# Kernel tuning notes

Hardware: AMD Instinct MI355X
Metric: run time of the kernel (lower is better)

The kernel has to match this reference:

```python
import jax, jax.numpy as jnp
import numpy as np

D_MODEL = 1024
N_HEAD = 16

def setup_inputs() -> dict:
    key = jax.random.key(0)
    ks = jax.random.split(key, 11)
    B, S, D = 2, 2048, D_MODEL
    s = 1.0 / np.sqrt(D)
    inp = {
        'q': jax.random.normal(ks[0], (B, S, D), jnp.float32),
        'k': jax.random.normal(ks[1], (B, S, D), jnp.float32),
        'v': jax.random.normal(ks[2], (B, S, D), jnp.float32),
        'w_q': jax.random.normal(ks[3], (D, D), jnp.float32) * s,
        'b_q': jnp.zeros((D,), jnp.float32),
        'w_k': jax.random.normal(ks[4], (D, D), jnp.float32) * s,
        'b_k': jnp.zeros((D,), jnp.float32),
        'w_v': jax.random.normal(ks[5], (D, D), jnp.float32) * s,
        'b_v': jnp.zeros((D,), jnp.float32),
        'w_o': jax.random.normal(ks[6], (D, D), jnp.float32) * s,
        'b_o': jnp.zeros((D,), jnp.float32),
    }
    return inp

def _split_heads(x):
    B, S, D = x.shape
    return x.reshape(B, S, N_HEAD, D // N_HEAD).transpose(0, 2, 1, 3)  # [B,H,S,d]

def reference(q, k, v, w_q, b_q, w_k, b_k, w_v, b_v, w_o, b_o):
    # Linear projections (torch Linear: x @ W.T + b)
    qh = _split_heads(q @ w_q.T + b_q)
    kh = _split_heads(k @ w_k.T + b_k)
    vh = _split_heads(v @ w_v.T + b_v)
    d_k = qh.shape[-1]
    scores = jnp.einsum('bhqd,bhkd->bhqk', qh, kh) / jnp.sqrt(jnp.float32(d_k))
    attn = jax.nn.softmax(scores, axis=-1)
    out = jnp.einsum('bhqk,bhkd->bhqd', attn, vh)  # [B,H,S,d]
    B, H, S, d = out.shape
    out = out.transpose(0, 2, 1, 3).reshape(B, S, H * d)
    return out @ w_o.T + b_o
```

## Files before the change

kernel.cpp:

```cpp
#include <hip/hip_runtime.h>
#include <hip/hip_bf16.h>

typedef __hip_bfloat16 bf16;
typedef short bf16x8 __attribute__((ext_vector_type(8)));
typedef float f32x4 __attribute__((ext_vector_type(4)));

#define D_MODEL 1024
#define SEQ     2048
#define NHEAD   16
#define DHEAD   64
#define BATCH   2
#define MROWS   (BATCH*SEQ)
#define LOG2E   1.4426950408889634f

__device__ __forceinline__ void lds_dma16(const bf16* g, bf16* l) {
  __builtin_amdgcn_global_load_lds(
      (const __attribute__((address_space(1))) void*)g,
      (__attribute__((address_space(3))) void*)l, 16, 0, 0);
}

__device__ __forceinline__ uint4 pack8_f32(const float4 x0, const float4 x1) {
  union { uint4 q; bf16 h[8]; } pk;
  pk.h[0]=__float2bfloat16(x0.x); pk.h[1]=__float2bfloat16(x0.y);
  pk.h[2]=__float2bfloat16(x0.z); pk.h[3]=__float2bfloat16(x0.w);
  pk.h[4]=__float2bfloat16(x1.x); pk.h[5]=__float2bfloat16(x1.y);
  pk.h[6]=__float2bfloat16(x1.z); pk.h[7]=__float2bfloat16(x1.w);
  return pk.q;
}

__global__ void probe_dtype(const void* __restrict__ w, int* __restrict__ flag) {
  __shared__ int cnt;
  const int tid = threadIdx.x;
  if (tid == 0) cnt = 0;
  __syncthreads();
  float v = ((const float*)w)[tid];
  bool sane = (v == v) && fabsf(v) < 1e3f && fabsf(v) > 1e-8f;
  if (sane) atomicAdd(&cnt, 1);
  __syncthreads();
  if (tid == 0) *flag = (cnt >= 128) ? 1 : 0;
}

__global__ __launch_bounds__(256) void convert7(
    const void* s0, const void* s1, const void* s2, const void* s3,
    const void* s4, const void* s5, const void* s6,
    bf16* d0, bf16* d1, bf16* d2, bf16* d3, bf16* d4, bf16* d5, bf16* d6,
    const int* __restrict__ dflag)
{
  const void* S[7] = {s0,s1,s2,s3,s4,s5,s6};
  bf16*       D[7] = {d0,d1,d2,d3,d4,d5,d6};
  const int z = blockIdx.y;
  const int n8 = (z < 3) ? (MROWS*D_MODEL/8) : (D_MODEL*D_MODEL/8);
  const bool is32 = (*dflag != 0);
  for (int i = blockIdx.x*256 + threadIdx.x; i < n8; i += 512*256) {
    if (is32) {
      float4 a = ((const float4*)S[z])[2*i];
      float4 b = ((const float4*)S[z])[2*i+1];
      ((uint4*)D[z])[i] = pack8_f32(a, b);
    } else {
      ((uint4*)D[z])[i] = ((const uint4*)S[z])[i];
    }
  }
}

__global__ __launch_bounds__(256) void gemm3_dma(
    const bf16* A0, const bf16* A1, const bf16* A2,
    const bf16* W0, const bf16* W1, const bf16* W2,
    const void* B0, const void* B1, const void* B2,
    bf16* C0, bf16* C1, bf16* C2, const int* __restrict__ dflag)
{
  __shared__ __align__(16) bf16 As[4*128*8];
  __shared__ __align__(16) bf16 Ws[4*128*8];
  const int z = blockIdx.z;
  const bf16* A = (z == 0) ? A0 : (z == 1) ? A1 : A2;
  const bf16* W = (z == 0) ? W0 : (z == 1) ? W1 : W2;
  const void* Bv = (z == 0) ? B0 : (z == 1) ? B1 : B2;
  bf16* C = (z == 0) ? C0 : (z == 1) ? C1 : C2;
  const float scale = (z == 0) ? 0.125f*LOG2E : 1.0f;
  const int K = D_MODEL, N = D_MODEL;
  const bool is32 = (*dflag != 0);
  const int tid  = threadIdx.x;
  const int lane = tid & 63, wave = tid >> 6;
  const int wm   = wave >> 1, wn = wave & 1;
  const int quad = lane >> 4, l16 = lane & 15;
  const int row0 = blockIdx.y * 128, col0 = blockIdx.x * 128;

  const f32x4 zero = {0.f, 0.f, 0.f, 0.f};
  f32x4 acc[4][4];
  #pragma unroll
  for (int i = 0; i < 4; ++i)
    #pragma unroll
    for (int j = 0; j < 4; ++j) acc[i][j] = zero;

  for (int k0 = 0; k0 < K; k0 += 32) {
    __syncthreads();
    #pragma unroll
    for (int t = 0; t < 2; ++t) {
      int s = t*256 + tid;
      int g = s >> 7, r = s & 127;
      lds_dma16(A + (size_t)(row0 + r)*K + k0 + g*8, &As[s*8]);
      lds_dma16(W + (size_t)(col0 + r)*K + k0 + g*8, &Ws[s*8]);
    }
    __syncthreads();
    bf16x8 af[4], wf[4];
    #pragma unroll
    for (int mt = 0; mt < 4; ++mt)
      af[mt] = *(const bf16x8*)&As[(quad*128 + wm*64 + mt*16 + l16)*8];
    #pragma unroll
    for (int nt = 0; nt < 4; ++nt)
      wf[nt] = *(const bf16x8*)&Ws[(quad*128 + wn*64 + nt*16 + l16)*8];
    #pragma unroll
    for (int mt = 0; mt < 4; ++mt)
      #pragma unroll
      for (int nt = 0; nt < 4; ++nt)
        acc[mt][nt] = __builtin_amdgcn_mfma_f32_16x16x32_bf16(af[mt], wf[nt], acc[mt][nt], 0, 0, 0);
  }

  #pragma unroll
  for (int nt = 0; nt < 4; ++nt) {
    int c = col0 + wn*64 + nt*16 + l16;
    float bv = is32 ? ((const float*)Bv)[c] : __bfloat162float(((const bf16*)Bv)[c]);
    #pragma unroll
    for (int mt = 0; mt < 4; ++mt) {
      int r = row0 + wm*64 + mt*16 + quad*4;
      #pragma unroll
      for (int j = 0; j < 4; ++j)
        C[(size_t)(r + j)*N + c] = __float2bfloat16((acc[mt][nt][j] + bv) * scale);
    }
  }
}

__global__ __launch_bounds__(256) void gemm_out_dma(
    const bf16* __restrict__ A, const bf16* __restrict__ W,
    const void* __restrict__ Bv, void* __restrict__ C,
    const int* __restrict__ dflag)
{
  __shared__ __align__(16) bf16 As[4*128*8];
  __shared__ __align__(16) bf16 Ws[4*64*8];
  const int K = D_MODEL, N = D_MODEL;
  const bool is32 = (*dflag != 0);
  const int tid  = threadIdx.x;
  const int lane = tid & 63, wave = tid >> 6;
  const int wm   = wave >> 1, wn = wave & 1;
  const int quad = lane >> 4, l16 = lane & 15;
  const int row0 = blockIdx.y * 128, col0 = blockIdx.x * 64;

  const f32x4 zero = {0.f, 0.f, 0.f, 0.f};
  f32x4 acc[4][2];
  #pragma unroll
  for (int i = 0; i < 4; ++i)
    #pragma unroll
    for (int j = 0; j < 2; ++j) acc[i][j] = zero;

  for (int k0 = 0; k0 < K; k0 += 32) {
    __syncthreads();
    #pragma unroll
    for (int t = 0; t < 2; ++t) {
      int s = t*256 + tid;
      int g = s >> 7, r = s & 127;
      lds_dma16(A + (size_t)(row0 + r)*K + k0 + g*8, &As[s*8]);
    }
    {
      int g = tid >> 6, r = tid & 63;
      lds_dma16(W + (size_t)(col0 + r)*K + k0 + g*8, &Ws[tid*8]);
    }
    __syncthreads();
    bf16x8 af[4], wf[2];
    #pragma unroll
    for (int mt = 0; mt < 4; ++mt)
      af[mt] = *(const bf16x8*)&As[(quad*128 + wm*64 + mt*16 + l16)*8];
    #pragma unroll
    for (int nt = 0; nt < 2; ++nt)
      wf[nt] = *(const bf16x8*)&Ws[(quad*64 + wn*32 + nt*16 + l16)*8];
    #pragma unroll
    for (int mt = 0; mt < 4; ++mt)
      #pragma unroll
      for (int nt = 0; nt < 2; ++nt)
        acc[mt][nt] = __builtin_amdgcn_mfma_f32_16x16x32_bf16(af[mt], wf[nt], acc[mt][nt], 0, 0, 0);
  }

  #pragma unroll
  for (int nt = 0; nt < 2; ++nt) {
    int c = col0 + wn*32 + nt*16 + l16;
    float bv = is32 ? ((const float*)Bv)[c] : __bfloat162float(((const bf16*)Bv)[c]);
    #pragma unroll
    for (int mt = 0; mt < 4; ++mt) {
      int r = row0 + wm*64 + mt*16 + quad*4;
      #pragma unroll
      for (int j = 0; j < 4; ++j) {
        float outv = acc[mt][nt][j] + bv;
        size_t idx = (size_t)(r + j)*N + c;
        if (is32) ((float*)C)[idx] = outv;
        else      ((bf16*)C)[idx]  = __float2bfloat16(outv);
      }
    }
  }
}

__global__ __launch_bounds__(256) void gemm3_fused(
    const void* A0, const void* A1, const void* A2,
    const void* W0, const void* W1, const void* W2,
    const void* B0, const void* B1, const void* B2,
    bf16* C0, bf16* C1, bf16* C2, const int* __restrict__ dflag)
{
  __shared__ __align__(16) bf16 As[4*128*8];
  __shared__ __align__(16) bf16 Ws[4*128*8];
  const int z = blockIdx.z;
  const void* A = (z == 0) ? A0 : (z == 1) ? A1 : A2;
  const void* W = (z == 0) ? W0 : (z == 1) ? W1 : W2;
  const void* Bv = (z == 0) ? B0 : (z == 1) ? B1 : B2;
  bf16* C = (z == 0) ? C0 : (z == 1) ? C1 : C2;
  const float scale = (z == 0) ? 0.125f*LOG2E : 1.0f;
  const int K = D_MODEL, N = D_MODEL;
  const bool is32 = (*dflag != 0);
  const int tid  = threadIdx.x;
  const int lane = tid & 63, wave = tid >> 6;
  const int wm   = wave >> 1, wn = wave & 1;
  const int quad = lane >> 4, l16 = lane & 15;
  const int row0 = blockIdx.y * 128, col0 = blockIdx.x * 128;

  const f32x4 zero = {0.f, 0.f, 0.f, 0.f};
  f32x4 acc[4][4];
  #pragma unroll
  for (int i = 0; i < 4; ++i)
    #pragma unroll
    for (int j = 0; j < 4; ++j) acc[i][j] = zero;

  for (int k0 = 0; k0 < K; k0 += 32) {
    __syncthreads();
    #pragma unroll
    for (int t = 0; t < 2; ++t) {
      int s = t*256 + tid;
      int g = s >> 7, r = s & 127;
      size_t offA = (size_t)(row0 + r)*K + k0 + g*8;
      size_t offW = (size_t)(col0 + r)*K + k0 + g*8;
      if (is32) {
        const float* Af = (const float*)A + offA;
        *(uint4*)&As[s*8] = pack8_f32(((const float4*)Af)[0], ((const float4*)Af)[1]);
        const float* Wf = (const float*)W + offW;
        *(uint4*)&Ws[s*8] = pack8_f32(((const float4*)Wf)[0], ((const float4*)Wf)[1]);
      } else {
        *(uint4*)&As[s*8] = *(const uint4*)((const bf16*)A + offA);
        *(uint4*)&Ws[s*8] = *(const uint4*)((const bf16*)W + offW);
      }
    }
    __syncthreads();
    bf16x8 af[4], wf[4];
    #pragma unroll
    for (int mt = 0; mt < 4; ++mt)
      af[mt] = *(const bf16x8*)&As[(quad*128 + wm*64 + mt*16 + l16)*8];
    #pragma unroll
    for (int nt = 0; nt < 4; ++nt)
      wf[nt] = *(const bf16x8*)&Ws[(quad*128 + wn*64 + nt*16 + l16)*8];
    #pragma unroll
    for (int mt = 0; mt < 4; ++mt)
      #pragma unroll
      for (int nt = 0; nt < 4; ++nt)
        acc[mt][nt] = __builtin_amdgcn_mfma_f32_16x16x32_bf16(af[mt], wf[nt], acc[mt][nt], 0, 0, 0);
  }
  #pragma unroll
  for (int nt = 0; nt < 4; ++nt) {
    int c = col0 + wn*64 + nt*16 + l16;
    float bv = is32 ? ((const float*)Bv)[c] : __bfloat162float(((const bf16*)Bv)[c]);
    #pragma unroll
    for (int mt = 0; mt < 4; ++mt) {
      int r = row0 + wm*64 + mt*16 + quad*4;
      #pragma unroll
      for (int j = 0; j < 4; ++j)
        C[(size_t)(r + j)*N + c] = __float2bfloat16((acc[mt][nt][j] + bv) * scale);
    }
  }
}

__global__ __launch_bounds__(256) void gemm_out_fused(
    const bf16* __restrict__ A, const void* __restrict__ W,
    const void* __restrict__ Bv, void* __restrict__ C,
    const int* __restrict__ dflag)
{
  __shared__ __align__(16) bf16 As[4*128*8];
  __shared__ __align__(16) bf16 Ws[4*64*8];
  const int K = D_MODEL, N = D_MODEL;
  const bool is32 = (*dflag != 0);
  const int tid  = threadIdx.x;
  const int lane = tid & 63, wave = tid >> 6;
  const int wm   = wave >> 1, wn = wave & 1;
  const int quad = lane >> 4, l16 = lane & 15;
  const int row0 = blockIdx.y * 128, col0 = blockIdx.x * 64;

  const f32x4 zero = {0.f, 0.f, 0.f, 0.f};
  f32x4 acc[4][2];
  #pragma unroll
  for (int i = 0; i < 4; ++i)
    #pragma unroll
    for (int j = 0; j < 2; ++j) acc[i][j] = zero;

  for (int k0 = 0; k0 < K; k0 += 32) {
    __syncthreads();
    #pragma unroll
    for (int t = 0; t < 2; ++t) {
      int s = t*256 + tid;
      int g = s >> 7, r = s & 127;
      *(uint4*)&As[s*8] = *(const uint4*)(A + (size_t)(row0 + r)*K + k0 + g*8);
    }
    {
      int g = tid >> 6, r = tid & 63;
      size_t offW = (size_t)(col0 + r)*K + k0 + g*8;
      if (is32) {
        const float* Wf = (const float*)W + offW;
        *(uint4*)&Ws[tid*8] = pack8_f32(((const float4*)Wf)[0], ((const float4*)Wf)[1]);
      } else {
        *(uint4*)&Ws[tid*8] = *(const uint4*)((const bf16*)W + offW);
      }
    }
    __syncthreads();
    bf16x8 af[4], wf[2];
    #pragma unroll
    for (int mt = 0; mt < 4; ++mt)
      af[mt] = *(const bf16x8*)&As[(quad*128 + wm*64 + mt*16 + l16)*8];
    #pragma unroll
    for (int nt = 0; nt < 2; ++nt)
      wf[nt] = *(const bf16x8*)&Ws[(quad*64 + wn*32 + nt*16 + l16)*8];
    #pragma unroll
    for (int mt = 0; mt < 4; ++mt)
      #pragma unroll
      for (int nt = 0; nt < 2; ++nt)
        acc[mt][nt] = __builtin_amdgcn_mfma_f32_16x16x32_bf16(af[mt], wf[nt], acc[mt][nt], 0, 0, 0);
  }
  #pragma unroll
  for (int nt = 0; nt < 2; ++nt) {
    int c = col0 + wn*32 + nt*16 + l16;
    float bv = is32 ? ((const float*)Bv)[c] : __bfloat162float(((const bf16*)Bv)[c]);
    #pragma unroll
    for (int mt = 0; mt < 4; ++mt) {
      int r = row0 + wm*64 + mt*16 + quad*4;
      #pragma unroll
      for (int j = 0; j < 4; ++j) {
        float outv = acc[mt][nt][j] + bv;
        size_t idx = (size_t)(r + j)*N + c;
        if (is32) ((float*)C)[idx] = outv;
        else      ((bf16*)C)[idx]  = __float2bfloat16(outv);
      }
    }
  }
}

__global__ __launch_bounds__(512, 4) void attn_fused(
    const bf16* __restrict__ Qp, const bf16* __restrict__ Kp,
    const bf16* __restrict__ Vp, bf16* __restrict__ Ao)
{
  __shared__ __align__(16) bf16 UN[128*128];
  __shared__ __align__(16) bf16 Ks[8*128*8];
  __shared__ __align__(16) bf16 Vt[64*16*8];

  const int tid  = threadIdx.x;
  const int lane = tid & 63, wave = tid >> 6;
  const int quad = lane >> 4, l16 = lane & 15;
  const int qt = blockIdx.x, h = blockIdx.y, b = blockIdx.z;
  const int q0 = qt * 128;
  const bf16* Qb = Qp + ((size_t)b*SEQ + q0)*D_MODEL + h*DHEAD;
  const bf16* Kb = Kp + (size_t)b*SEQ*D_MODEL + h*DHEAD;
  const bf16* Vb = Vp + (size_t)b*SEQ*D_MODEL + h*DHEAD;

  #pragma unroll
  for (int t = 0; t < 2; ++t) {
    int s = t*512 + tid;
    int g = s >> 7, r = s & 127;
    lds_dma16(Qb + (size_t)r*D_MODEL + g*8, &UN[s*8]);
  }
  __syncthreads();

  const int wq0 = wave * 16;
  const int q   = wq0 + l16;
  bf16x8 qa[2];
  #pragma unroll
  for (int ks = 0; ks < 2; ++ks)
    qa[ks] = *(const bf16x8*)&UN[((ks*4 + quad)*128 + q)*8];
  __syncthreads();
  bf16* Ps = UN;
  const int swz = (l16 & 7) << 1;

  const f32x4 zero = {0.f, 0.f, 0.f, 0.f};
  f32x4 acc_o[4];
  #pragma unroll
  for (int dt = 0; dt < 4; ++dt) acc_o[dt] = zero;
  float m_s = -1e30f, l_s = 0.f;

  for (int kt = 0; kt < SEQ/128; ++kt) {
    const bf16* Kt_ = Kb + (size_t)kt*128*D_MODEL;
    const bf16* Vs_ = Vb + (size_t)kt*128*D_MODEL;
    #pragma unroll
    for (int t = 0; t < 2; ++t) {
      int s = t*512 + tid;
      int g = s >> 7, kk = s & 127;
      lds_dma16(Kt_ + (size_t)kk*D_MODEL + g*8, &Ks[s*8]);
    }
    #pragma unroll
    for (int t = 0; t < 2; ++t) {
      int c = t*512 + tid;
      int key = c >> 3, g8 = c & 7;
      uint4 raw = *(const uint4*)(Vs_ + (size_t)key*D_MODEL + g8*8);
      const bf16* e = (const bf16*)&raw;
      int gk = key >> 3, kb_i = key & 7;
      #pragma unroll
      for (int i = 0; i < 8; ++i) {
        int n = g8*8 + i;
        int sw = (gk + n + (n >> 3)) & 15;
        Vt[(n*16 + sw)*8 + kb_i] = e[i];
      }
    }
    __syncthreads();

    f32x4 sc[8];
    #pragma unroll
    for (int kt2 = 0; kt2 < 8; ++kt2) sc[kt2] = zero;
    #pragma unroll
    for (int ks = 0; ks < 2; ++ks) {
      bf16x8 kf[8];
      #pragma unroll
      for (int kt2 = 0; kt2 < 8; ++kt2)
        kf[kt2] = *(const bf16x8*)&Ks[((ks*4 + quad)*128 + kt2*16 + l16)*8];
      #pragma unroll
      for (int kt2 = 0; kt2 < 8; ++kt2)
        sc[kt2] = __builtin_amdgcn_mfma_f32_16x16x32_bf16(kf[kt2], qa[ks], sc[kt2], 0, 0, 0);
    }

    float vmax = -1e30f;
    #pragma unroll
    for (int kt2 = 0; kt2 < 8; ++kt2) {
      f32x4 s4 = sc[kt2];
      vmax = fmaxf(vmax, fmaxf(fmaxf(s4[0], s4[1]), fmaxf(s4[2], s4[3])));
    }
    vmax = fmaxf(vmax, __shfl_xor(vmax, 16));
    vmax = fmaxf(vmax, __shfl_xor(vmax, 32));
    float mnew  = fmaxf(m_s, vmax);
    float alpha = __builtin_amdgcn_exp2f(m_s - mnew);
    float rs = 0.f;
    #pragma unroll
    for (int kt2 = 0; kt2 < 8; ++kt2) {
      float p0 = __builtin_amdgcn_exp2f(sc[kt2][0] - mnew);
      float p1 = __builtin_amdgcn_exp2f(sc[kt2][1] - mnew);
      float p2 = __builtin_amdgcn_exp2f(sc[kt2][2] - mnew);
      float p3 = __builtin_amdgcn_exp2f(sc[kt2][3] - mnew);
      rs += (p0 + p1) + (p2 + p3);
      union { uint2 u; bf16 hh[4]; } pk;
      pk.hh[0] = __float2bfloat16(p0); pk.hh[1] = __float2bfloat16(p1);
      pk.hh[2] = __float2bfloat16(p2); pk.hh[3] = __float2bfloat16(p3);
      int phys = (kt2*4 + quad) ^ swz;
      *(uint2*)&Ps[q*128 + phys*4] = pk.u;
    }
    rs += __shfl_xor(rs, 16);
    rs += __shfl_xor(rs, 32);
    l_s = l_s*alpha + rs;
    m_s = mnew;
    #pragma unroll
    for (int dt = 0; dt < 4; ++dt) acc_o[dt] = acc_o[dt] * alpha;

    #pragma unroll
    for (int ks2 = 0; ks2 < 4; ++ks2) {
      bf16x8 vf[4], pa;
      #pragma unroll
      for (int dt = 0; dt < 4; ++dt) {
        int n = dt*16 + l16;
        int sw = (ks2*4 + quad + n + (n >> 3)) & 15;
        vf[dt] = *(const bf16x8*)&Vt[(n*16 + sw)*8];
      }
      int phys = (ks2*8 + quad*2) ^ swz;
      pa = *(const bf16x8*)&Ps[q*128 + phys*4];
      #pragma unroll
      for (int dt = 0; dt < 4; ++dt)
        acc_o[dt] = __builtin_amdgcn_mfma_f32_16x16x32_bf16(vf[dt], pa, acc_o[dt], 0, 0, 0);
    }
    __syncthreads();
  }

  bf16* Ob = Ao + ((size_t)b*SEQ + q0)*D_MODEL + h*DHEAD;
  float inv = 1.f / l_s;
  #pragma unroll
  for (int dt = 0; dt < 4; ++dt) {
    union { uint2 u; bf16 hh[4]; } pk;
    #pragma unroll
    for (int j = 0; j < 4; ++j) pk.hh[j] = __float2bfloat16(acc_o[dt][j] * inv);
    *(uint2*)(Ob + (size_t)q*D_MODEL + dt*16 + quad*4) = pk.u;
  }
}

extern "C" void kernel_launch(void* const* d_in, const int* in_sizes, int n_in,
                              void* d_out, int out_size, void* d_ws, size_t ws_size,
                              hipStream_t stream) {
  const void* q   = d_in[0];
  const void* k   = d_in[1];
  const void* v   = d_in[2];
  const void* w_q = d_in[3];
  const void* b_q = d_in[4];
  const void* w_k = d_in[5];
  const void* b_k = d_in[6];
  const void* w_v = d_in[7];
  const void* b_v = d_in[8];
  const void* w_o = d_in[9];
  const void* b_o = d_in[10];

  const size_t nbuf  = (size_t)MROWS * D_MODEL;
  const size_t wbuf  = (size_t)D_MODEL * D_MODEL;
  int* flag = (int*)d_ws;

  dim3 blk(256);
  probe_dtype<<<1, 256, 0, stream>>>(w_q, flag);

  const size_t needA = 256 + 3*nbuf*2 + 4*wbuf*2 + nbuf*2;
  if (ws_size >= needA) {
    bf16* qc  = (bf16*)((char*)d_ws + 256);
    bf16* kc  = qc  + nbuf;
    bf16* vc  = kc  + nbuf;
    bf16* wqc = vc  + nbuf;
    bf16* wkc = wqc + wbuf;
    bf16* wvc = wkc + wbuf;
    bf16* woc = wvc + wbuf;
    bf16* Qp  = woc + wbuf;
    bf16* Kp  = (bf16*)d_out;
    bf16* Vp  = Kp + nbuf;
    bf16* Ao  = Qp;

    dim3 gc(512, 7);
    convert7<<<gc, blk, 0, stream>>>(q, k, v, w_q, w_k, w_v, w_o,
                                     qc, kc, vc, wqc, wkc, wvc, woc, flag);
    dim3 g3(D_MODEL/128, MROWS/128, 3);
    gemm3_dma<<<g3, blk, 0, stream>>>(qc, kc, vc, wqc, wkc, wvc,
                                      b_q, b_k, b_v, Qp, Kp, Vp, flag);
    dim3 ga(SEQ/128, NHEAD, BATCH);
    attn_fused<<<ga, dim3(512), 0, stream>>>(Qp, Kp, Vp, Ao);
    dim3 go(D_MODEL/64, MROWS/128);
    gemm_out_dma<<<go, blk, 0, stream>>>(Ao, woc, b_o, d_out, flag);
  } else {
    bf16* Qp = (bf16*)((char*)d_ws + 256);
    bf16* Vp = Qp + nbuf;
    bf16* Kp = (bf16*)d_out;
    bf16* Ao = Qp;
    dim3 g3(D_MODEL/128, MROWS/128, 3);
    gemm3_fused<<<g3, blk, 0, stream>>>(q, k, v, w_q, w_k, w_v,
                                        b_q, b_k, b_v, Qp, Kp, Vp, flag);
    dim3 ga(SEQ/128, NHEAD, BATCH);
    attn_fused<<<ga, dim3(512), 0, stream>>>(Qp, Kp, Vp, Ao);
    dim3 go(D_MODEL/64, MROWS/128);
    gemm_out_fused<<<go, blk, 0, stream>>>(Ao, w_o, b_o, d_out, flag);
  }
}
```

Measured before the change: 314.1 us.

## Write V projection transposed, double GEMM K-step, drop dtype probe

The V projection epilogue now writes V in a transposed [batch, feature, seq] layout. The attention kernel can then load V rows with vector loads straight into the swizzled LDS tile instead of scattering single elements. The DMA GEMMs stage 64-wide K chunks per barrier pair instead of 32, halving the number of syncs. The runtime dtype probe kernel and its flag branches are removed by assuming fp32 inputs, and the attention kernel's launch-bounds occupancy hint is dropped. The costs are larger LDS tiles and transposed stores from the GEMM epilogue that are only partially coalesced.

```diff
diff --git a/kernel.cpp b/kernel.cpp
--- a/kernel.cpp
+++ b/kernel.cpp
@@ -28,56 +28,35 @@
   return pk.q;
 }
 
-__global__ void probe_dtype(const void* __restrict__ w, int* __restrict__ flag) {
-  __shared__ int cnt;
-  const int tid = threadIdx.x;
-  if (tid == 0) cnt = 0;
-  __syncthreads();
-  float v = ((const float*)w)[tid];
-  bool sane = (v == v) && fabsf(v) < 1e3f && fabsf(v) > 1e-8f;
-  if (sane) atomicAdd(&cnt, 1);
-  __syncthreads();
-  if (tid == 0) *flag = (cnt >= 128) ? 1 : 0;
-}
-
 __global__ __launch_bounds__(256) void convert7(
-    const void* s0, const void* s1, const void* s2, const void* s3,
-    const void* s4, const void* s5, const void* s6,
-    bf16* d0, bf16* d1, bf16* d2, bf16* d3, bf16* d4, bf16* d5, bf16* d6,
-    const int* __restrict__ dflag)
+    const float* s0, const float* s1, const float* s2, const float* s3,
+    const float* s4, const float* s5, const float* s6,
+    bf16* d0, bf16* d1, bf16* d2, bf16* d3, bf16* d4, bf16* d5, bf16* d6)
 {
-  const void* S[7] = {s0,s1,s2,s3,s4,s5,s6};
-  bf16*       D[7] = {d0,d1,d2,d3,d4,d5,d6};
+  const float* S[7] = {s0,s1,s2,s3,s4,s5,s6};
+  bf16*        D[7] = {d0,d1,d2,d3,d4,d5,d6};
   const int z = blockIdx.y;
   const int n8 = (z < 3) ? (MROWS*D_MODEL/8) : (D_MODEL*D_MODEL/8);
-  const bool is32 = (*dflag != 0);
   for (int i = blockIdx.x*256 + threadIdx.x; i < n8; i += 512*256) {
-    if (is32) {
-      float4 a = ((const float4*)S[z])[2*i];
-      float4 b = ((const float4*)S[z])[2*i+1];
-      ((uint4*)D[z])[i] = pack8_f32(a, b);
-    } else {
-      ((uint4*)D[z])[i] = ((const uint4*)S[z])[i];
-    }
+    float4 a = ((const float4*)S[z])[2*i];
+    float4 b = ((const float4*)S[z])[2*i+1];
+    ((uint4*)D[z])[i] = pack8_f32(a, b);
   }
 }
 
 __global__ __launch_bounds__(256) void gemm3_dma(
     const bf16* A0, const bf16* A1, const bf16* A2,
     const bf16* W0, const bf16* W1, const bf16* W2,
-    const void* B0, const void* B1, const void* B2,
-    bf16* C0, bf16* C1, bf16* C2, const int* __restrict__ dflag)
+    const float* B0, const float* B1, const float* B2,
+    bf16* C0, bf16* C1, bf16* VpT)
 {
-  __shared__ __align__(16) bf16 As[4*128*8];
-  __shared__ __align__(16) bf16 Ws[4*128*8];
+  __shared__ __align__(16) bf16 As[8*128*8];
+  __shared__ __align__(16) bf16 Ws[8*128*8];
   const int z = blockIdx.z;
   const bf16* A = (z == 0) ? A0 : (z == 1) ? A1 : A2;
   const bf16* W = (z == 0) ? W0 : (z == 1) ? W1 : W2;
-  const void* Bv = (z == 0) ? B0 : (z == 1) ? B1 : B2;
-  bf16* C = (z == 0) ? C0 : (z == 1) ? C1 : C2;
-  const float scale = (z == 0) ? 0.125f*LOG2E : 1.0f;
+  const float* Bv = (z == 0) ? B0 : (z == 1) ? B1 : B2;
   const int K = D_MODEL, N = D_MODEL;
-  const bool is32 = (*dflag != 0);
   const int tid  = threadIdx.x;
   const int lane = tid & 63, wave = tid >> 6;
   const int wm   = wave >> 1, wn = wave & 1;
@@ -91,53 +70,75 @@
     #pragma unroll
     for (int j = 0; j < 4; ++j) acc[i][j] = zero;
 
-  for (int k0 = 0; k0 < K; k0 += 32) {
-    __syncthreads();
-    #pragma unroll
-    for (int t = 0; t < 2; ++t) {
+  for (int k0 = 0; k0 < K; k0 += 64) {
+    __syncthreads();
+    #pragma unroll
+    for (int t = 0; t < 4; ++t) {
       int s = t*256 + tid;
       int g = s >> 7, r = s & 127;
       lds_dma16(A + (size_t)(row0 + r)*K + k0 + g*8, &As[s*8]);
       lds_dma16(W + (size_t)(col0 + r)*K + k0 + g*8, &Ws[s*8]);
     }
     __syncthreads();
-    bf16x8 af[4], wf[4];
-    #pragma unroll
-    for (int mt = 0; mt < 4; ++mt)
-      af[mt] = *(const bf16x8*)&As[(quad*128 + wm*64 + mt*16 + l16)*8];
-    #pragma unroll
-    for (int nt = 0; nt < 4; ++nt)
-      wf[nt] = *(const bf16x8*)&Ws[(quad*128 + wn*64 + nt*16 + l16)*8];
-    #pragma unroll
-    for (int mt = 0; mt < 4; ++mt)
+    #pragma unroll
+    for (int ks = 0; ks < 2; ++ks) {
+      bf16x8 af[4], wf[4];
+      #pragma unroll
+      for (int mt = 0; mt < 4; ++mt)
+        af[mt] = *(const bf16x8*)&As[((ks*4 + quad)*128 + wm*64 + mt*16 + l16)*8];
       #pragma unroll
       for (int nt = 0; nt < 4; ++nt)
-        acc[mt][nt] = __builtin_amdgcn_mfma_f32_16x16x32_bf16(af[mt], wf[nt], acc[mt][nt], 0, 0, 0);
-  }
-
-  #pragma unroll
-  for (int nt = 0; nt < 4; ++nt) {
-    int c = col0 + wn*64 + nt*16 + l16;
-    float bv = is32 ? ((const float*)Bv)[c] : __bfloat162float(((const bf16*)Bv)[c]);
-    #pragma unroll
-    for (int mt = 0; mt < 4; ++mt) {
-      int r = row0 + wm*64 + mt*16 + quad*4;
-      #pragma unroll
-      for (int j = 0; j < 4; ++j)
-        C[(size_t)(r + j)*N + c] = __float2bfloat16((acc[mt][nt][j] + bv) * scale);
+        wf[nt] = *(const bf16x8*)&Ws[((ks*4 + quad)*128 + wn*64 + nt*16 + l16)*8];
+      #pragma unroll
+      for (int mt = 0; mt < 4; ++mt)
+        #pragma unroll
+        for (int nt = 0; nt < 4; ++nt)
+          acc[mt][nt] = __builtin_amdgcn_mfma_f32_16x16x32_bf16(af[mt], wf[nt], acc[mt][nt], 0, 0, 0);
+    }
+  }
+
+  if (z < 2) {
+    bf16* C = (z == 0) ? C0 : C1;
+    const float scale = (z == 0) ? 0.125f*LOG2E : 1.0f;
+    #pragma unroll
+    for (int nt = 0; nt < 4; ++nt) {
+      int c = col0 + wn*64 + nt*16 + l16;
+      float bv = Bv[c];
+      #pragma unroll
+      for (int mt = 0; mt < 4; ++mt) {
+        int r = row0 + wm*64 + mt*16 + quad*4;
+        #pragma unroll
+        for (int j = 0; j < 4; ++j)
+          C[(size_t)(r + j)*N + c] = __float2bfloat16((acc[mt][nt][j] + bv) * scale);
+      }
+    }
+  } else {
+    const int bb = row0 >> 11;
+    const int sbase = (row0 & 2047) + wm*64;
+    #pragma unroll
+    for (int nt = 0; nt < 4; ++nt) {
+      int c = col0 + wn*64 + nt*16 + l16;
+      float bv = Bv[c];
+      bf16* col = VpT + (size_t)((bb << 10) + c) * SEQ;
+      #pragma unroll
+      for (int mt = 0; mt < 4; ++mt) {
+        int s = sbase + mt*16 + quad*4;
+        union { uint2 u; bf16 h[4]; } pk;
+        #pragma unroll
+        for (int j = 0; j < 4; ++j) pk.h[j] = __float2bfloat16(acc[mt][nt][j] + bv);
+        *(uint2*)(col + s) = pk.u;
+      }
     }
   }
 }
 
 __global__ __launch_bounds__(256) void gemm_out_dma(
     const bf16* __restrict__ A, const bf16* __restrict__ W,
-    const void* __restrict__ Bv, void* __restrict__ C,
-    const int* __restrict__ dflag)
+    const float* __restrict__ Bv, float* __restrict__ C)
 {
-  __shared__ __align__(16) bf16 As[4*128*8];
-  __shared__ __align__(16) bf16 Ws[4*64*8];
+  __shared__ __align__(16) bf16 As[8*128*8];
+  __shared__ __align__(16) bf16 Ws[8*64*8];
   const int K = D_MODEL, N = D_MODEL;
-  const bool is32 = (*dflag != 0);
   const int tid  = threadIdx.x;
   const int lane = tid & 63, wave = tid >> 6;
   const int wm   = wave >> 1, wn = wave & 1;
@@ -151,67 +152,65 @@
     #pragma unroll
     for (int j = 0; j < 2; ++j) acc[i][j] = zero;
 
-  for (int k0 = 0; k0 < K; k0 += 32) {
-    __syncthreads();
-    #pragma unroll
-    for (int t = 0; t < 2; ++t) {
+  for (int k0 = 0; k0 < K; k0 += 64) {
+    __syncthreads();
+    #pragma unroll
+    for (int t = 0; t < 4; ++t) {
       int s = t*256 + tid;
       int g = s >> 7, r = s & 127;
       lds_dma16(A + (size_t)(row0 + r)*K + k0 + g*8, &As[s*8]);
     }
-    {
-      int g = tid >> 6, r = tid & 63;
-      lds_dma16(W + (size_t)(col0 + r)*K + k0 + g*8, &Ws[tid*8]);
-    }
-    __syncthreads();
-    bf16x8 af[4], wf[2];
-    #pragma unroll
-    for (int mt = 0; mt < 4; ++mt)
-      af[mt] = *(const bf16x8*)&As[(quad*128 + wm*64 + mt*16 + l16)*8];
-    #pragma unroll
-    for (int nt = 0; nt < 2; ++nt)
-      wf[nt] = *(const bf16x8*)&Ws[(quad*64 + wn*32 + nt*16 + l16)*8];
-    #pragma unroll
-    for (int mt = 0; mt < 4; ++mt)
+    #pragma unroll
+    for (int t = 0; t < 2; ++t) {
+      int s = t*256 + tid;
+      int g = s >> 6, r = s & 63;
+      lds_dma16(W + (size_t)(col0 + r)*K + k0 + g*8, &Ws[s*8]);
+    }
+    __syncthreads();
+    #pragma unroll
+    for (int ks = 0; ks < 2; ++ks) {
+      bf16x8 af[4], wf[2];
+      #pragma unroll
+      for (int mt = 0; mt < 4; ++mt)
+        af[mt] = *(const bf16x8*)&As[((ks*4 + quad)*128 + wm*64 + mt*16 + l16)*8];
       #pragma unroll
       for (int nt = 0; nt < 2; ++nt)
-        acc[mt][nt] = __builtin_amdgcn_mfma_f32_16x16x32_bf16(af[mt], wf[nt], acc[mt][nt], 0, 0, 0);
+        wf[nt] = *(const bf16x8*)&Ws[((ks*4 + quad)*64 + wn*32 + nt*16 + l16)*8];
+      #pragma unroll
+      for (int mt = 0; mt < 4; ++mt)
+        #pragma unroll
+        for (int nt = 0; nt < 2; ++nt)
+          acc[mt][nt] = __builtin_amdgcn_mfma_f32_16x16x32_bf16(af[mt], wf[nt], acc[mt][nt], 0, 0, 0);
+    }
   }
 
   #pragma unroll
   for (int nt = 0; nt < 2; ++nt) {
     int c = col0 + wn*32 + nt*16 + l16;
-    float bv = is32 ? ((const float*)Bv)[c] : __bfloat162float(((const bf16*)Bv)[c]);
+    float bv = Bv[c];
     #pragma unroll
     for (int mt = 0; mt < 4; ++mt) {
       int r = row0 + wm*64 + mt*16 + quad*4;
       #pragma unroll
-      for (int j = 0; j < 4; ++j) {
-        float outv = acc[mt][nt][j] + bv;
-        size_t idx = (size_t)(r + j)*N + c;
-        if (is32) ((float*)C)[idx] = outv;
-        else      ((bf16*)C)[idx]  = __float2bfloat16(outv);
-      }
+      for (int j = 0; j < 4; ++j)
+        C[(size_t)(r + j)*N + c] = acc[mt][nt][j] + bv;
     }
   }
 }
 
 __global__ __launch_bounds__(256) void gemm3_fused(
-    const void* A0, const void* A1, const void* A2,
-    const void* W0, const void* W1, const void* W2,
-    const void* B0, const void* B1, const void* B2,
-    bf16* C0, bf16* C1, bf16* C2, const int* __restrict__ dflag)
+    const float* A0, const float* A1, const float* A2,
+    const float* W0, const float* W1, const float* W2,
+    const float* B0, const float* B1, const float* B2,
+    bf16* C0, bf16* C1, bf16* VpT)
 {
   __shared__ __align__(16) bf16 As[4*128*8];
   __shared__ __align__(16) bf16 Ws[4*128*8];
   const int z = blockIdx.z;
-  const void* A = (z == 0) ? A0 : (z == 1) ? A1 : A2;
-  const void* W = (z == 0) ? W0 : (z == 1) ? W1 : W2;
-  const void* Bv = (z == 0) ? B0 : (z == 1) ? B1 : B2;
-  bf16* C = (z == 0) ? C0 : (z == 1) ? C1 : C2;
-  const float scale = (z == 0) ? 0.125f*LOG2E : 1.0f;
+  const float* A = (z == 0) ? A0 : (z == 1) ? A1 : A2;
+  const float* W = (z == 0) ? W0 : (z == 1) ? W1 : W2;
+  const float* Bv = (z == 0) ? B0 : (z == 1) ? B1 : B2;
   const int K = D_MODEL, N = D_MODEL;
-  const bool is32 = (*dflag != 0);
   const int tid  = threadIdx.x;
   const int lane = tid & 63, wave = tid >> 6;
   const int wm   = wave >> 1, wn = wave & 1;
@@ -231,17 +230,10 @@
     for (int t = 0; t < 2; ++t) {
       int s = t*256 + tid;
       int g = s >> 7, r = s & 127;
-      size_t offA = (size_t)(row0 + r)*K + k0 + g*8;
-      size_t offW = (size_t)(col0 + r)*K + k0 + g*8;
-      if (is32) {
-        const float* Af = (const float*)A + offA;
-        *(uint4*)&As[s*8] = pack8_f32(((const float4*)Af)[0], ((const float4*)Af)[1]);
-        const float* Wf = (const float*)W + offW;
-        *(uint4*)&Ws[s*8] = pack8_f32(((const float4*)Wf)[0], ((const float4*)Wf)[1]);
-      } else {
-        *(uint4*)&As[s*8] = *(const uint4*)((const bf16*)A + offA);
-        *(uint4*)&Ws[s*8] = *(const uint4*)((const bf16*)W + offW);
-      }
+      const float* Af = A + (size_t)(row0 + r)*K + k0 + g*8;
+      *(uint4*)&As[s*8] = pack8_f32(((const float4*)Af)[0], ((const float4*)Af)[1]);
+      const float* Wf = W + (size_t)(col0 + r)*K + k0 + g*8;
+      *(uint4*)&Ws[s*8] = pack8_f32(((const float4*)Wf)[0], ((const float4*)Wf)[1]);
     }
     __syncthreads();
     bf16x8 af[4], wf[4];
@@ -257,29 +249,49 @@
       for (int nt = 0; nt < 4; ++nt)
         acc[mt][nt] = __builtin_amdgcn_mfma_f32_16x16x32_bf16(af[mt], wf[nt], acc[mt][nt], 0, 0, 0);
   }
-  #pragma unroll
-  for (int nt = 0; nt < 4; ++nt) {
-    int c = col0 + wn*64 + nt*16 + l16;
-    float bv = is32 ? ((const float*)Bv)[c] : __bfloat162float(((const bf16*)Bv)[c]);
-    #pragma unroll
-    for (int mt = 0; mt < 4; ++mt) {
-      int r = row0 + wm*64 + mt*16 + quad*4;
-      #pragma unroll
-      for (int j = 0; j < 4; ++j)
-        C[(size_t)(r + j)*N + c] = __float2bfloat16((acc[mt][nt][j] + bv) * scale);
+
+  if (z < 2) {
+    bf16* C = (z == 0) ? C0 : C1;
+    const float scale = (z == 0) ? 0.125f*LOG2E : 1.0f;
+    #pragma unroll
+    for (int nt = 0; nt < 4; ++nt) {
+      int c = col0 + wn*64 + nt*16 + l16;
+      float bv = Bv[c];
+      #pragma unroll
+      for (int mt = 0; mt < 4; ++mt) {
+        int r = row0 + wm*64 + mt*16 + quad*4;
+        #pragma unroll
+        for (int j = 0; j < 4; ++j)
+          C[(size_t)(r + j)*N + c] = __float2bfloat16((acc[mt][nt][j] + bv) * scale);
+      }
+    }
+  } else {
+    const int bb = row0 >> 11;
+    const int sbase = (row0 & 2047) + wm*64;
+    #pragma unroll
+    for (int nt = 0; nt < 4; ++nt) {
+      int c = col0 + wn*64 + nt*16 + l16;
+      float bv = Bv[c];
+      bf16* col = VpT + (size_t)((bb << 10) + c) * SEQ;
+      #pragma unroll
+      for (int mt = 0; mt < 4; ++mt) {
+        int s = sbase + mt*16 + quad*4;
+        union { uint2 u; bf16 h[4]; } pk;
+        #pragma unroll
+        for (int j = 0; j < 4; ++j) pk.h[j] = __float2bfloat16(acc[mt][nt][j] + bv);
+        *(uint2*)(col + s) = pk.u;
+      }
     }
   }
 }
 
 __global__ __launch_bounds__(256) void gemm_out_fused(
-    const bf16* __restrict__ A, const void* __restrict__ W,
-    const void* __restrict__ Bv, void* __restrict__ C,
-    const int* __restrict__ dflag)
+    const bf16* __restrict__ A, const float* __restrict__ W,
+    const float* __restrict__ Bv, float* __restrict__ C)
 {
   __shared__ __align__(16) bf16 As[4*128*8];
   __shared__ __align__(16) bf16 Ws[4*64*8];
   const int K = D_MODEL, N = D_MODEL;
-  const bool is32 = (*dflag != 0);
   const int tid  = threadIdx.x;
   const int lane = tid & 63, wave = tid >> 6;
   const int wm   = wave >> 1, wn = wave & 1;
@@ -303,13 +315,8 @@
     }
     {
       int g = tid >> 6, r = tid & 63;
-      size_t offW = (size_t)(col0 + r)*K + k0 + g*8;
-      if (is32) {
-        const float* Wf = (const float*)W + offW;
-        *(uint4*)&Ws[tid*8] = pack8_f32(((const float4*)Wf)[0], ((const float4*)Wf)[1]);
-      } else {
-        *(uint4*)&Ws[tid*8] = *(const uint4*)((const bf16*)W + offW);
-      }
+      const float* Wf = W + (size_t)(col0 + r)*K + k0 + g*8;
+      *(uint4*)&Ws[tid*8] = pack8_f32(((const float4*)Wf)[0], ((const float4*)Wf)[1]);
     }
     __syncthreads();
     bf16x8 af[4], wf[2];
@@ -328,24 +335,20 @@
   #pragma unroll
   for (int nt = 0; nt < 2; ++nt) {
     int c = col0 + wn*32 + nt*16 + l16;
-    float bv = is32 ? ((const float*)Bv)[c] : __bfloat162float(((const bf16*)Bv)[c]);
+    float bv = Bv[c];
     #pragma unroll
     for (int mt = 0; mt < 4; ++mt) {
       int r = row0 + wm*64 + mt*16 + quad*4;
       #pragma unroll
-      for (int j = 0; j < 4; ++j) {
-        float outv = acc[mt][nt][j] + bv;
-        size_t idx = (size_t)(r + j)*N + c;
-        if (is32) ((float*)C)[idx] = outv;
-        else      ((bf16*)C)[idx]  = __float2bfloat16(outv);
-      }
-    }
-  }
-}
-
-__global__ __launch_bounds__(512, 4) void attn_fused(
+      for (int j = 0; j < 4; ++j)
+        C[(size_t)(r + j)*N + c] = acc[mt][nt][j] + bv;
+    }
+  }
+}
+
+__global__ __launch_bounds__(512) void attn_fused(
     const bf16* __restrict__ Qp, const bf16* __restrict__ Kp,
-    const bf16* __restrict__ Vp, bf16* __restrict__ Ao)
+    const bf16* __restrict__ VpT, bf16* __restrict__ Ao)
 {
   __shared__ __align__(16) bf16 UN[128*128];
   __shared__ __align__(16) bf16 Ks[8*128*8];
@@ -358,7 +361,7 @@
   const int q0 = qt * 128;
   const bf16* Qb = Qp + ((size_t)b*SEQ + q0)*D_MODEL + h*DHEAD;
   const bf16* Kb = Kp + (size_t)b*SEQ*D_MODEL + h*DHEAD;
-  const bf16* Vb = Vp + (size_t)b*SEQ*D_MODEL + h*DHEAD;
+  const bf16* Vg = VpT + (size_t)((b << 10) + h*DHEAD) * SEQ;
 
   #pragma unroll
   for (int t = 0; t < 2; ++t) {
@@ -385,27 +388,19 @@
   float m_s = -1e30f, l_s = 0.f;
 
   for (int kt = 0; kt < SEQ/128; ++kt) {
-    const bf16* Kt_ = Kb + (size_t)kt*128*D_MODEL;
-    const bf16* Vs_ = Vb + (size_t)kt*128*D_MODEL;
     #pragma unroll
     for (int t = 0; t < 2; ++t) {
       int s = t*512 + tid;
       int g = s >> 7, kk = s & 127;
-      lds_dma16(Kt_ + (size_t)kk*D_MODEL + g*8, &Ks[s*8]);
+      lds_dma16(Kb + (size_t)(kt*128 + kk)*D_MODEL + g*8, &Ks[s*8]);
     }
     #pragma unroll
     for (int t = 0; t < 2; ++t) {
       int c = t*512 + tid;
-      int key = c >> 3, g8 = c & 7;
-      uint4 raw = *(const uint4*)(Vs_ + (size_t)key*D_MODEL + g8*8);
-      const bf16* e = (const bf16*)&raw;
-      int gk = key >> 3, kb_i = key & 7;
-      #pragma unroll
-      for (int i = 0; i < 8; ++i) {
-        int n = g8*8 + i;
-        int sw = (gk + n + (n >> 3)) & 15;
-        Vt[(n*16 + sw)*8 + kb_i] = e[i];
-      }
+      int n = c >> 4, gk = c & 15;
+      uint4 raw = *(const uint4*)(Vg + (size_t)n*SEQ + kt*128 + gk*8);
+      int sw = (gk + n + (n >> 3)) & 15;
+      *(uint4*)&Vt[(n*16 + sw)*8] = raw;
     }
     __syncthreads();
 
@@ -486,26 +481,24 @@
 extern "C" void kernel_launch(void* const* d_in, const int* in_sizes, int n_in,
                               void* d_out, int out_size, void* d_ws, size_t ws_size,
                               hipStream_t stream) {
-  const void* q   = d_in[0];
-  const void* k   = d_in[1];
-  const void* v   = d_in[2];
-  const void* w_q = d_in[3];
-  const void* b_q = d_in[4];
-  const void* w_k = d_in[5];
-  const void* b_k = d_in[6];
-  const void* w_v = d_in[7];
-  const void* b_v = d_in[8];
-  const void* w_o = d_in[9];
-  const void* b_o = d_in[10];
-
-  const size_t nbuf  = (size_t)MROWS * D_MODEL;
-  const size_t wbuf  = (size_t)D_MODEL * D_MODEL;
-  int* flag = (int*)d_ws;
-
-  dim3 blk(256);
-  probe_dtype<<<1, 256, 0, stream>>>(w_q, flag);
-
-  const size_t needA = 256 + 3*nbuf*2 + 4*wbuf*2 + nbuf*2;
+  const float* q   = (const float*)d_in[0];
+  const float* k   = (const float*)d_in[1];
+  const float* v   = (const float*)d_in[2];
+  const float* w_q = (const float*)d_in[3];
+  const float* b_q = (const float*)d_in[4];
+  const float* w_k = (const float*)d_in[5];
+  const float* b_k = (const float*)d_in[6];
+  const float* w_v = (const float*)d_in[7];
+  const float* b_v = (const float*)d_in[8];
+  const float* w_o = (const float*)d_in[9];
+  const float* b_o = (const float*)d_in[10];
+
+  const size_t nbuf = (size_t)MROWS * D_MODEL;
+  const size_t wbuf = (size_t)D_MODEL * D_MODEL;
+  bf16* Kp  = (bf16*)d_out;
+  bf16* VpT = Kp + nbuf;
+
+  const size_t needA = 256 + (3*nbuf + 4*wbuf + nbuf) * 2;
   if (ws_size >= needA) {
     bf16* qc  = (bf16*)((char*)d_ws + 256);
     bf16* kc  = qc  + nbuf;
@@ -515,31 +508,20 @@
     bf16* wvc = wkc + wbuf;
     bf16* woc = wvc + wbuf;
     bf16* Qp  = woc + wbuf;
-    bf16* Kp  = (bf16*)d_out;
-    bf16* Vp  = Kp + nbuf;
     bf16* Ao  = Qp;
 
-    dim3 gc(512, 7);
-    convert7<<<gc, blk, 0, stream>>>(q, k, v, w_q, w_k, w_v, w_o,
-                                     qc, kc, vc, wqc, wkc, wvc, woc, flag);
-    dim3 g3(D_MODEL/128, MROWS/128, 3);
-    gemm3_dma<<<g3, blk, 0, stream>>>(qc, kc, vc, wqc, wkc, wvc,
-                                      b_q, b_k, b_v, Qp, Kp, Vp, flag);
-    dim3 ga(SEQ/128, NHEAD, BATCH);
-    attn_fused<<<ga, dim3(512), 0, stream>>>(Qp, Kp, Vp, Ao);
-    dim3 go(D_MODEL/64, MROWS/128);
-    gemm_out_dma<<<go, blk, 0, stream>>>(Ao, woc, b_o, d_out, flag);
+    convert7<<<dim3(512,7), 256, 0, stream>>>(q, k, v, w_q, w_k, w_v, w_o,
+                                              qc, kc, vc, wqc, wkc, wvc, woc);
+    gemm3_dma<<<dim3(8,32,3), 256, 0, stream>>>(qc, kc, vc, wqc, wkc, wvc,
+                                                b_q, b_k, b_v, Qp, Kp, VpT);
+    attn_fused<<<dim3(16,16,2), 512, 0, stream>>>(Qp, Kp, VpT, Ao);
+    gemm_out_dma<<<dim3(16,32), 256, 0, stream>>>(Ao, woc, b_o, (float*)d_out);
   } else {
     bf16* Qp = (bf16*)((char*)d_ws + 256);
-    bf16* Vp = Qp + nbuf;
-    bf16* Kp = (bf16*)d_out;
     bf16* Ao = Qp;
-    dim3 g3(D_MODEL/128, MROWS/128, 3);
-    gemm3_fused<<<g3, blk, 0, stream>>>(q, k, v, w_q, w_k, w_v,
-                                        b_q, b_k, b_v, Qp, Kp, Vp, flag);
-    dim3 ga(SEQ/128, NHEAD, BATCH);
-    attn_fused<<<ga, dim3(512), 0, stream>>>(Qp, Kp, Vp, Ao);
-    dim3 go(D_MODEL/64, MROWS/128);
-    gemm_out_fused<<<go, blk, 0, stream>>>(Ao, w_o, b_o, d_out, flag);
-  }
-}
+    gemm3_fused<<<dim3(8,32,3), 256, 0, stream>>>(q, k, v, w_q, w_k, w_v,
+                                                  b_q, b_k, b_v, Qp, Kp, VpT);
+    attn_fused<<<dim3(16,16,2), 512, 0, stream>>>(Qp, Kp, VpT, Ao);
+    gemm_out_fused<<<dim3(16,32), 256, 0, stream>>>(Ao, w_o, b_o, (float*)d_out);
+  }
+}
```

Measured after the change: 309.7 us. About the same (-1.4%).
